# Kernel tuning notes

Hardware: AMD Instinct MI355X
Metric: run time of the kernel (lower is better)

## Reference

```python
import jax, jax.numpy as jnp
import numpy as np

B, N, E, D, R, M, L = 8, 8192, 16384, 128, 200, 20, 3


def setup_inputs() -> dict:
    key = jax.random.key(0)
    ks = jax.random.split(key, 16)
    return {
        "dists": jax.random.randint(ks[0], (B, N), 0, 10),
        "edge_index": jax.random.randint(ks[1], (B, 2, E), 0, N),
        "rels": jax.random.randint(ks[2], (B, E), 0, R),
        "node_mask": jax.random.randint(ks[3], (B, N), 0, 2).astype(bool),
        "edge_mask": jax.random.randint(ks[4], (B, E), 0, 2).astype(bool),
        "r_query_embed": jax.random.normal(ks[5], (B, D), dtype=jnp.float32),
        "conf_embeds": jax.random.normal(ks[6], (B, E, D), dtype=jnp.float32),
        "noise": jax.random.normal(ks[7], (B, N, D), dtype=jnp.float32),
        "dist_table": jax.random.normal(ks[8], (10, D), dtype=jnp.float32) * 0.02,
        "rel_table": jax.random.normal(ks[9], (R, D), dtype=jnp.float32) * 0.02,
        "msg_W": jax.random.normal(ks[10], (L, 5 * D, D), dtype=jnp.float32) / np.sqrt(5 * D),
        "msg_b": jnp.zeros((L, D), jnp.float32),
        "upd_W": jax.random.normal(ks[11], (L, D, D), dtype=jnp.float32) / np.sqrt(D),
        "upd_b": jnp.zeros((L, D), jnp.float32),
        "att_W": jax.random.normal(ks[12], (2 * D, 1), dtype=jnp.float32) / np.sqrt(2 * D),
        "att_b": jnp.zeros((1,), jnp.float32),
    }


def reference(dists, edge_index, rels, node_mask, edge_mask, r_query_embed,
              conf_embeds, noise, dist_table, rel_table, msg_W, msg_b,
              upd_W, upd_b, att_W, att_b):
    dist_emb = dist_table[jnp.clip(dists, 0, 9)]            # [B,N,D]
    h = dist_emb + noise * 0.1
    src = edge_index[:, 0, :]                               # [B,E]
    tgt = edge_index[:, 1, :]                               # [B,E]
    em = edge_mask[..., None].astype(h.dtype)               # [B,E,1]
    h_r = rel_table[rels]                                   # [B,E,D]
    dist_src = jnp.take_along_axis(dist_emb, src[..., None], axis=1)  # [B,E,D]

    def scatter_add(t_idx, msg):
        return jnp.zeros((N, D), msg.dtype).at[t_idx].add(msg)

    for k in range(L):
        h_src = jnp.take_along_axis(h, src[..., None], axis=1)        # [B,E,D]
        comp = h_src * h_r
        msg_in = jnp.concatenate([comp, h_src, dist_src, h_r, conf_embeds], axis=-1)  # [B,E,5D]
        msg = jax.nn.relu(jnp.einsum('bef,fd->bed', msg_in, msg_W[k]) + msg_b[k]) * em
        aggr = jax.vmap(scatter_add)(tgt, msg)                        # [B,N,D]
        h = jnp.einsum('bnd,df->bnf', aggr, upd_W[k]) + upd_b[k] + h

    h = h * node_mask[..., None].astype(h.dtype)
    t_state = h[:, 0, :]
    r_q = jnp.broadcast_to(r_query_embed[:, None, :], (B, N, D))
    att_in = jnp.concatenate([h, r_q], axis=-1)                       # [B,N,2D]
    scores = jax.nn.leaky_relu((att_in @ att_W + att_b)[..., 0], 0.01)
    scores = jnp.where(node_mask, scores, -1e9)
    alpha = jax.nn.softmax(scores, axis=1)
    topk_vals, topk_idx = jax.lax.top_k(alpha, M)                     # [B,M]
    H_evd = jnp.take_along_axis(h, topk_idx[..., None], axis=1) * topk_vals[..., None]
    return (H_evd, t_state)
```

## Files before the change

### kernel.cpp

```cpp
#include <hip/hip_runtime.h>
#include <hip/hip_bf16.h>
#include <math.h>

#define B_ 8
#define N_ 8192
#define E_ 16384
#define D_ 128
#define R_ 200
#define M_ 20
#define L_ 3
#define KEFF 384
#define LDA 392
#define LDU 136

typedef __attribute__((ext_vector_type(8))) short bf16x8;
typedef __attribute__((ext_vector_type(4))) float f32x4;

__device__ __forceinline__ short f2b(float f) {
  union { __hip_bfloat16 b; short s; } u;
  u.b = __float2bfloat16(f);
  return u.s;
}
__device__ __forceinline__ bf16x8 pack8(float4 x, float4 y) {
  bf16x8 r;
  r[0] = f2b(x.x); r[1] = f2b(x.y); r[2] = f2b(x.z); r[3] = f2b(x.w);
  r[4] = f2b(y.x); r[5] = f2b(y.y); r[6] = f2b(y.z); r[7] = f2b(y.w);
  return r;
}
__device__ __forceinline__ bf16x8 pack8mul(float4 x, float4 rx, float4 y, float4 ry) {
  bf16x8 r;
  r[0] = f2b(x.x * rx.x); r[1] = f2b(x.y * rx.y); r[2] = f2b(x.z * rx.z); r[3] = f2b(x.w * rx.w);
  r[4] = f2b(y.x * ry.x); r[5] = f2b(y.y * ry.y); r[6] = f2b(y.z * ry.z); r[7] = f2b(y.w * ry.w);
  return r;
}

__global__ __launch_bounds__(256) void k_init_h(const int* __restrict__ dists,
    const float* __restrict__ noise, const float* __restrict__ dist_table,
    float* __restrict__ h) {
  int i = blockIdx.x * 256 + threadIdx.x;
  int row = i >> 5;
  int d4 = i & 31;
  int dc = dists[row]; dc = dc < 0 ? 0 : (dc > 9 ? 9 : dc);
  const float4 t = *(const float4*)&dist_table[dc * D_ + d4 * 4];
  const float4 nz = *(const float4*)&noise[(size_t)i * 4];
  float4 o;
  o.x = t.x + 0.1f * nz.x; o.y = t.y + 0.1f * nz.y;
  o.z = t.z + 0.1f * nz.z; o.w = t.w + 0.1f * nz.w;
  *(float4*)&h[(size_t)i * 4] = o;
}

__global__ __launch_bounds__(256) void k_compact(const int* __restrict__ edge_mask,
    int* __restrict__ count, int* __restrict__ list) {
  int i = blockIdx.x * 256 + threadIdx.x;
  bool act = edge_mask[i] != 0;
  unsigned long long m = __ballot(act);
  int lane = threadIdx.x & 63;
  int base = 0;
  if (lane == 0) base = atomicAdd(count, __popcll(m));
  base = __shfl(base, 0);
  if (act) list[base + __popcll(m & ((1ull << lane) - 1ull))] = i;
}

__global__ __launch_bounds__(128) void k_tables(const float* __restrict__ dist_table,
    const float* __restrict__ rel_table, const float* __restrict__ msg_W,
    const float* __restrict__ msg_b, float* __restrict__ T3b, float* __restrict__ T4) {
  int k = blockIdx.x / 210;
  int r = blockIdx.x % 210;
  int d = threadIdx.x;
  if (r < 10) {
    float acc = msg_b[k * D_ + d];
    for (int f = 0; f < D_; ++f)
      acc = fmaf(dist_table[r * D_ + f], msg_W[(size_t)(k * 640 + 256 + f) * D_ + d], acc);
    T3b[(k * 10 + r) * D_ + d] = acc;
  } else {
    int rr = r - 10;
    float acc = 0.f;
    for (int f = 0; f < D_; ++f)
      acc = fmaf(rel_table[rr * D_ + f], msg_W[(size_t)(k * 640 + 384 + f) * D_ + d], acc);
    T4[(k * R_ + rr) * D_ + d] = acc;
  }
}

__global__ __launch_bounds__(256) void k_wbt_msg(const float* __restrict__ msg_W,
    short* __restrict__ Wbt) {
  int idx = blockIdx.x * 256 + threadIdx.x;
  int fe = idx % KEFF;
  int t = idx / KEFF;
  int n = t & 127;
  int k = t >> 7;
  int row = fe < 256 ? fe : fe + 256;
  Wbt[idx] = f2b(msg_W[(size_t)(k * 640 + row) * D_ + n]);
}

__global__ __launch_bounds__(256) void k_wbt_upd(const float* __restrict__ upd_W,
    short* __restrict__ Wbt) {
  int idx = blockIdx.x * 256 + threadIdx.x;
  int f = idx & 127;
  int t = idx >> 7;
  int n = t & 127;
  int k = t >> 7;
  Wbt[idx] = f2b(upd_W[(size_t)(k * D_ + f) * D_ + n]);
}

__global__ __launch_bounds__(256, 3) void k_msg(
    const int* __restrict__ count_p, const int* __restrict__ list,
    const int* __restrict__ edge_index, const int* __restrict__ rels,
    const int* __restrict__ dists, const float* __restrict__ h,
    const float* __restrict__ rel_table, const float* __restrict__ conf,
    const short* __restrict__ Wbt,
    const float* __restrict__ T3b,
    const float* __restrict__ T4,
    float* __restrict__ aggr) {
  int cnt = *count_p;
  int base = blockIdx.x * 64;
  if (base >= cnt) return;
  int ne = min(64, cnt - base);
  __shared__ __align__(16) short sA[64 * LDA];
  __shared__ int sMeta[64][5];
  int tid = threadIdx.x;
  if (tid < 64) {
    int t = tid < ne ? tid : 0;
    int id = list[base + t];
    int b = id >> 14;
    int e = id & (E_ - 1);
    int src = edge_index[(b * 2) * E_ + e];
    int tgt = edge_index[(b * 2 + 1) * E_ + e];
    int dc = dists[b * N_ + src];
    dc = dc < 0 ? 0 : (dc > 9 ? 9 : dc);
    sMeta[tid][0] = b * N_ + src;
    sMeta[tid][1] = id;
    sMeta[tid][2] = b * N_ + tgt;
    sMeta[tid][3] = dc;
    sMeta[tid][4] = rels[id];
  }
  __syncthreads();
  {
    int i = tid >> 2, q = tid & 3;
    const float4* ph = (const float4*)(h + (size_t)sMeta[i][0] * D_ + q * 32);
    const float4* pr = (const float4*)(rel_table + (size_t)sMeta[i][4] * D_ + q * 32);
    const float4* pc = (const float4*)(conf + (size_t)sMeta[i][1] * D_ + q * 32);
    float4 hv[8], rv[8], cv[8];
#pragma unroll
    for (int j = 0; j < 8; ++j) hv[j] = ph[j];
#pragma unroll
    for (int j = 0; j < 8; ++j) rv[j] = pr[j];
#pragma unroll
    for (int j = 0; j < 8; ++j) cv[j] = pc[j];
    short* rowp = &sA[i * LDA];
#pragma unroll
    for (int j = 0; j < 4; ++j) {
      *(bf16x8*)&rowp[q * 32 + j * 8]       = pack8mul(hv[2*j], rv[2*j], hv[2*j+1], rv[2*j+1]);
      *(bf16x8*)&rowp[128 + q * 32 + j * 8] = pack8(hv[2*j], hv[2*j+1]);
      *(bf16x8*)&rowp[256 + q * 32 + j * 8] = pack8(cv[2*j], cv[2*j+1]);
    }
  }
  __syncthreads();
  int lane = tid & 63, wv = tid >> 6;
  int wm = wv >> 1, wn = wv & 1;
  int g = lane >> 4, cl = lane & 15;
  const short* pa0 = &sA[(wm * 32 + cl) * LDA];
  const short* pa1 = pa0 + 16 * LDA;
  const short* wb = Wbt + (size_t)(wn * 64 + cl) * KEFF;

  f32x4 acc[2][4];
  f32x4 zz = {0.f, 0.f, 0.f, 0.f};
#pragma unroll
  for (int tm = 0; tm < 2; ++tm)
#pragma unroll
    for (int tn = 0; tn < 4; ++tn) acc[tm][tn] = zz;

#pragma unroll
  for (int kstep = 0; kstep < 12; ++kstep) {
    int o = kstep * 32 + g * 8;
    bf16x8 a0 = *(const bf16x8*)&pa0[o];
    bf16x8 a1 = *(const bf16x8*)&pa1[o];
    const short* wk = wb + o;
    bf16x8 b0 = *(const bf16x8*)(wk);
    bf16x8 b1 = *(const bf16x8*)(wk + 16 * KEFF);
    bf16x8 b2 = *(const bf16x8*)(wk + 32 * KEFF);
    bf16x8 b3 = *(const bf16x8*)(wk + 48 * KEFF);
    acc[0][0] = __builtin_amdgcn_mfma_f32_16x16x32_bf16(a0, b0, acc[0][0], 0, 0, 0);
    acc[0][1] = __builtin_amdgcn_mfma_f32_16x16x32_bf16(a0, b1, acc[0][1], 0, 0, 0);
    acc[0][2] = __builtin_amdgcn_mfma_f32_16x16x32_bf16(a0, b2, acc[0][2], 0, 0, 0);
    acc[0][3] = __builtin_amdgcn_mfma_f32_16x16x32_bf16(a0, b3, acc[0][3], 0, 0, 0);
    acc[1][0] = __builtin_amdgcn_mfma_f32_16x16x32_bf16(a1, b0, acc[1][0], 0, 0, 0);
    acc[1][1] = __builtin_amdgcn_mfma_f32_16x16x32_bf16(a1, b1, acc[1][1], 0, 0, 0);
    acc[1][2] = __builtin_amdgcn_mfma_f32_16x16x32_bf16(a1, b2, acc[1][2], 0, 0, 0);
    acc[1][3] = __builtin_amdgcn_mfma_f32_16x16x32_bf16(a1, b3, acc[1][3], 0, 0, 0);
  }
#pragma unroll
  for (int tm = 0; tm < 2; ++tm)
#pragma unroll
    for (int reg = 0; reg < 4; ++reg) {
      int edge = wm * 32 + tm * 16 + g * 4 + reg;
      if (edge < ne) {
        int arow = sMeta[edge][2];
        int dc = sMeta[edge][3];
        int rl = sMeta[edge][4];
#pragma unroll
        for (int tn = 0; tn < 4; ++tn) {
          int n = wn * 64 + tn * 16 + cl;
          float bias = T3b[dc * D_ + n] + T4[rl * D_ + n];
          float vv = fmaxf(acc[tm][tn][reg] + bias, 0.f);
          unsafeAtomicAdd(&aggr[(size_t)arow * D_ + n], vv);
        }
      }
    }
}

__global__ __launch_bounds__(256, 4) void k_upd(
    float* __restrict__ aggr, const short* __restrict__ Wbt,
    const float* __restrict__ upd_b, float* __restrict__ h) {
  int base = blockIdx.x * 64;
  int tid = threadIdx.x;
  __shared__ __align__(16) short sU[64 * LDU];
  {
    int i = tid >> 2, q = tid & 3;
    float4* ap = (float4*)(aggr + (size_t)(base + i) * D_ + q * 32);
    float4 av[8];
    float4 z4 = make_float4(0.f, 0.f, 0.f, 0.f);
#pragma unroll
    for (int j = 0; j < 8; ++j) av[j] = ap[j];
#pragma unroll
    for (int j = 0; j < 8; ++j) ap[j] = z4;
    short* rowp = &sU[i * LDU];
#pragma unroll
    for (int j = 0; j < 4; ++j)
      *(bf16x8*)&rowp[q * 32 + j * 8] = pack8(av[2*j], av[2*j+1]);
  }
  __syncthreads();
  int lane = tid & 63, wv = tid >> 6;
  int wm = wv >> 1, wn = wv & 1;
  int g = lane >> 4, cl = lane & 15;
  const short* pa0 = &sU[(wm * 32 + cl) * LDU];
  const short* pa1 = pa0 + 16 * LDU;
  const short* wb = Wbt + (size_t)(wn * 64 + cl) * D_;

  f32x4 acc[2][4];
  f32x4 zz = {0.f, 0.f, 0.f, 0.f};
#pragma unroll
  for (int tm = 0; tm < 2; ++tm)
#pragma unroll
    for (int tn = 0; tn < 4; ++tn) acc[tm][tn] = zz;

#pragma unroll
  for (int kstep = 0; kstep < 4; ++kstep) {
    int o = kstep * 32 + g * 8;
    bf16x8 a0 = *(const bf16x8*)&pa0[o];
    bf16x8 a1 = *(const bf16x8*)&pa1[o];
    const short* wk = wb + o;
    bf16x8 b0 = *(const bf16x8*)(wk);
    bf16x8 b1 = *(const bf16x8*)(wk + 16 * D_);
    bf16x8 b2 = *(const bf16x8*)(wk + 32 * D_);
    bf16x8 b3 = *(const bf16x8*)(wk + 48 * D_);
    acc[0][0] = __builtin_amdgcn_mfma_f32_16x16x32_bf16(a0, b0, acc[0][0], 0, 0, 0);
    acc[0][1] = __builtin_amdgcn_mfma_f32_16x16x32_bf16(a0, b1, acc[0][1], 0, 0, 0);
    acc[0][2] = __builtin_amdgcn_mfma_f32_16x16x32_bf16(a0, b2, acc[0][2], 0, 0, 0);
    acc[0][3] = __builtin_amdgcn_mfma_f32_16x16x32_bf16(a0, b3, acc[0][3], 0, 0, 0);
    acc[1][0] = __builtin_amdgcn_mfma_f32_16x16x32_bf16(a1, b0, acc[1][0], 0, 0, 0);
    acc[1][1] = __builtin_amdgcn_mfma_f32_16x16x32_bf16(a1, b1, acc[1][1], 0, 0, 0);
    acc[1][2] = __builtin_amdgcn_mfma_f32_16x16x32_bf16(a1, b2, acc[1][2], 0, 0, 0);
    acc[1][3] = __builtin_amdgcn_mfma_f32_16x16x32_bf16(a1, b3, acc[1][3], 0, 0, 0);
  }
#pragma unroll
  for (int tm = 0; tm < 2; ++tm)
#pragma unroll
    for (int reg = 0; reg < 4; ++reg) {
      int grow = base + wm * 32 + tm * 16 + g * 4 + reg;
#pragma unroll
      for (int tn = 0; tn < 4; ++tn) {
        int n = wn * 64 + tn * 16 + cl;
        size_t gi = (size_t)grow * D_ + n;
        h[gi] = acc[tm][tn][reg] + upd_b[n] + h[gi];
      }
    }
}

__global__ __launch_bounds__(256) void k_score(const float* __restrict__ h,
    const int* __restrict__ node_mask, const float* __restrict__ r_query,
    const float* __restrict__ att_W, const float* __restrict__ att_b,
    float* __restrict__ sSg) {
  int wv = threadIdx.x >> 6, lane = threadIdx.x & 63;
  int node = blockIdx.x * 4 + wv;
  int b = node >> 13;
  float s;
  if (node_mask[node] == 0) {
    s = -1e9f;
  } else {
    float2 hv = *(const float2*)&h[(size_t)node * D_ + lane * 2];
    float2 w0 = *(const float2*)&att_W[lane * 2];
    float2 w1 = *(const float2*)&att_W[D_ + lane * 2];
    float2 rq = *(const float2*)&r_query[b * D_ + lane * 2];
    float v = hv.x * w0.x + hv.y * w0.y + rq.x * w1.x + rq.y * w1.y;
#pragma unroll
    for (int off = 32; off > 0; off >>= 1) v += __shfl_xor(v, off);
    v += att_b[0];
    s = v > 0.f ? v : 0.01f * v;
  }
  if (lane == 0) sSg[node] = s;
}

__global__ __launch_bounds__(1024) void k_top(const float* __restrict__ sSg,
    const float* __restrict__ h, const int* __restrict__ node_mask,
    float* __restrict__ out) {
  int b = blockIdx.x;
  int tid = threadIdx.x, lane = tid & 63, wv = tid >> 6;
  __shared__ float sS[N_];
  __shared__ float sRw[16];
  __shared__ float sSegV[16];
  __shared__ int sSegI[16];
  __shared__ float sTopV[M_];
  __shared__ int sTopI[M_];
  __shared__ float sMax, sSum;
  const float4* gp = (const float4*)&sSg[(size_t)b * N_];
#pragma unroll
  for (int r = 0; r < 2; ++r) {
    float4 x = gp[tid + r * 1024];
    *(float4*)&sS[(tid + r * 1024) * 4] = x;
  }
  __syncthreads();
  float lm = -INFINITY;
  for (int n = tid; n < N_; n += 1024) lm = fmaxf(lm, sS[n]);
#pragma unroll
  for (int off = 32; off > 0; off >>= 1) lm = fmaxf(lm, __shfl_xor(lm, off));
  if (lane == 0) sRw[wv] = lm;
  __syncthreads();
  if (tid == 0) {
    float m = sRw[0];
    for (int i = 1; i < 16; ++i) m = fmaxf(m, sRw[i]);
    sMax = m;
  }
  __syncthreads();
  float mx = sMax;
  float ls = 0.f;
  for (int n = tid; n < N_; n += 1024) ls += expf(sS[n] - mx);
#pragma unroll
  for (int off = 32; off > 0; off >>= 1) ls += __shfl_xor(ls, off);
  if (lane == 0) sRw[wv] = ls;
  __syncthreads();
  if (tid == 0) {
    float s = 0.f;
    for (int i = 0; i < 16; ++i) s += sRw[i];
    sSum = s;
  }
  {
    float bv = -INFINITY; int bi = 0;
    int s0 = wv * 512;
    for (int t2 = 0; t2 < 8; ++t2) {
      int n = s0 + lane + t2 * 64;
      float x = sS[n];
      if (x > bv) { bv = x; bi = n; }
    }
#pragma unroll
    for (int off = 32; off > 0; off >>= 1) {
      float vv = __shfl_xor(bv, off); int ii = __shfl_xor(bi, off);
      if (vv > bv || (vv == bv && ii < bi)) { bv = vv; bi = ii; }
    }
    if (lane == 0) { sSegV[wv] = bv; sSegI[wv] = bi; }
  }
  __syncthreads();
  for (int j = 0; j < M_; ++j) {
    if (wv == 0) {
      float bv = (lane < 16) ? sSegV[lane] : -INFINITY;
      int bi = (lane < 16) ? sSegI[lane] : 0x7fffffff;
#pragma unroll
      for (int off = 32; off > 0; off >>= 1) {
        float vv = __shfl_xor(bv, off); int ii = __shfl_xor(bi, off);
        if (vv > bv || (vv == bv && ii < bi)) { bv = vv; bi = ii; }
      }
      if (lane == 0) { sTopV[j] = bv; sTopI[j] = bi; sS[bi] = -INFINITY; }
    }
    __syncthreads();
    int seg = sTopI[j] >> 9;
    if (wv == seg) {
      float bv = -INFINITY; int bi = 0;
      int s0 = wv * 512;
      for (int t2 = 0; t2 < 8; ++t2) {
        int n = s0 + lane + t2 * 64;
        float x = sS[n];
        if (x > bv) { bv = x; bi = n; }
      }
#pragma unroll
      for (int off = 32; off > 0; off >>= 1) {
        float vv = __shfl_xor(bv, off); int ii = __shfl_xor(bi, off);
        if (vv > bv || (vv == bv && ii < bi)) { bv = vv; bi = ii; }
      }
      if (lane == 0) { sSegV[wv] = bv; sSegI[wv] = bi; }
    }
    __syncthreads();
  }
  float sum = sSum;
  if (tid < D_) {
    float vv = node_mask[b * N_] ? h[(size_t)b * N_ * D_ + tid] : 0.f;
    out[B_ * M_ * D_ + b * D_ + tid] = vv;
  }
  for (int s2 = tid; s2 < M_ * D_; s2 += 1024) {
    int j = s2 >> 7, d = s2 & 127;
    int idx = sTopI[j];
    float alpha = expf(sTopV[j] - mx) / sum;
    float hv = h[((size_t)b * N_ + idx) * D_ + d];
    if (!node_mask[b * N_ + idx]) hv = 0.f;
    out[(b * M_ + j) * D_ + d] = hv * alpha;
  }
}

extern "C" void kernel_launch(void* const* d_in, const int* in_sizes, int n_in,
                              void* d_out, int out_size, void* d_ws, size_t ws_size,
                              hipStream_t stream) {
  const int*   dists      = (const int*)d_in[0];
  const int*   edge_index = (const int*)d_in[1];
  const int*   rels       = (const int*)d_in[2];
  const int*   node_mask  = (const int*)d_in[3];
  const int*   edge_mask  = (const int*)d_in[4];
  const float* r_query    = (const float*)d_in[5];
  const float* conf       = (const float*)d_in[6];
  const float* noise      = (const float*)d_in[7];
  const float* dist_table = (const float*)d_in[8];
  const float* rel_table  = (const float*)d_in[9];
  const float* msg_W      = (const float*)d_in[10];
  const float* msg_b      = (const float*)d_in[11];
  const float* upd_W      = (const float*)d_in[12];
  const float* upd_b      = (const float*)d_in[13];
  const float* att_W      = (const float*)d_in[14];
  const float* att_b      = (const float*)d_in[15];
  float* out = (float*)d_out;

  char* ws = (char*)d_ws;
  size_t off = 0;
  auto alloc = [&](size_t bytes) {
    void* p = ws + off;
    off = (off + bytes + 255) & ~(size_t)255;
    return p;
  };
  int*   count   = (int*)alloc(4);
  int*   list    = (int*)alloc((size_t)B_ * E_ * 4);
  float* h       = (float*)alloc((size_t)B_ * N_ * D_ * 4);
  float* aggr    = (float*)alloc((size_t)B_ * N_ * D_ * 4);
  short* Wbt_msg = (short*)alloc((size_t)L_ * D_ * KEFF * 2);
  short* Wbt_upd = (short*)alloc((size_t)L_ * D_ * D_ * 2);
  float* T3b     = (float*)alloc((size_t)L_ * 10 * D_ * 4);
  float* T4      = (float*)alloc((size_t)L_ * R_ * D_ * 4);
  float* scores  = (float*)alloc((size_t)B_ * N_ * 4);
  (void)ws_size; (void)in_sizes; (void)n_in; (void)out_size;

  hipMemsetAsync(count, 0, 4, stream);
  hipMemsetAsync(aggr, 0, (size_t)B_ * N_ * D_ * 4, stream);

  k_init_h<<<B_ * N_ * D_ / 4 / 256, 256, 0, stream>>>(dists, noise, dist_table, h);
  k_compact<<<B_ * E_ / 256, 256, 0, stream>>>(edge_mask, count, list);
  k_tables<<<L_ * 210, 128, 0, stream>>>(dist_table, rel_table, msg_W, msg_b, T3b, T4);
  k_wbt_msg<<<L_ * D_ * KEFF / 256, 256, 0, stream>>>(msg_W, Wbt_msg);
  k_wbt_upd<<<L_ * D_ * D_ / 256, 256, 0, stream>>>(upd_W, Wbt_upd);

  for (int k = 0; k < L_; ++k) {
    k_msg<<<B_ * E_ / 64, 256, 0, stream>>>(count, list, edge_index, rels, dists, h,
        rel_table, conf, Wbt_msg + (size_t)k * D_ * KEFF,
        T3b + k * 10 * D_, T4 + k * R_ * D_, aggr);
    k_upd<<<B_ * N_ / 64, 256, 0, stream>>>(aggr, Wbt_upd + (size_t)k * D_ * D_,
        upd_b + k * D_, h);
  }
  k_score<<<B_ * N_ / 4, 256, 0, stream>>>(h, node_mask, r_query, att_W, att_b, scores);
  k_top<<<B_, 1024, 0, stream>>>(scores, h, node_mask, out);
}
```

Baseline: 544.6 us.

## Replace atomic scatter-add with CSR gather of per-edge messages

Instead of each message being atomically added into a dense aggr buffer, k_msg now writes per-edge messages to a buffer. k_upd then gathers them by target node through a CSR built once, using a count, a three-kernel prefix scan and an atomic fill. This removes the float atomics and the per-layer zeroing of the 16MB aggr buffer. In exchange it writes and reads a 64MB message buffer per layer, adds several setup kernels, and gives an irregular per-thread loop over in-degree.

```diff
diff --git a/kernel.cpp b/kernel.cpp
--- a/kernel.cpp
+++ b/kernel.cpp
@@ -50,7 +50,8 @@
 }
 
 __global__ __launch_bounds__(256) void k_compact(const int* __restrict__ edge_mask,
-    int* __restrict__ count, int* __restrict__ list) {
+    const int* __restrict__ edge_index, int* __restrict__ count,
+    int* __restrict__ list, int* __restrict__ cnt) {
   int i = blockIdx.x * 256 + threadIdx.x;
   bool act = edge_mask[i] != 0;
   unsigned long long m = __ballot(act);
@@ -58,7 +59,69 @@
   int base = 0;
   if (lane == 0) base = atomicAdd(count, __popcll(m));
   base = __shfl(base, 0);
-  if (act) list[base + __popcll(m & ((1ull << lane) - 1ull))] = i;
+  if (act) {
+    list[base + __popcll(m & ((1ull << lane) - 1ull))] = i;
+    int b = i >> 14, e = i & (E_ - 1);
+    int tgt = edge_index[(b * 2 + 1) * E_ + e];
+    atomicAdd(&cnt[b * N_ + tgt], 1);
+  }
+}
+
+__global__ __launch_bounds__(256) void k_scanA(const int* __restrict__ cnt,
+    int* __restrict__ bsum) {
+  __shared__ int s[4];
+  int v = cnt[blockIdx.x * 256 + threadIdx.x];
+#pragma unroll
+  for (int o = 32; o > 0; o >>= 1) v += __shfl_xor(v, o);
+  if ((threadIdx.x & 63) == 0) s[threadIdx.x >> 6] = v;
+  __syncthreads();
+  if (threadIdx.x == 0) bsum[blockIdx.x] = s[0] + s[1] + s[2] + s[3];
+}
+
+__global__ __launch_bounds__(256) void k_scanB(const int* __restrict__ bsum,
+    int* __restrict__ boff) {
+  __shared__ int s[256];
+  int t = threadIdx.x;
+  s[t] = bsum[t];
+  __syncthreads();
+  for (int o = 1; o < 256; o <<= 1) {
+    int v = (t >= o) ? s[t - o] : 0;
+    __syncthreads();
+    s[t] += v;
+    __syncthreads();
+  }
+  boff[t] = (t == 0) ? 0 : s[t - 1];
+}
+
+__global__ __launch_bounds__(256) void k_scanC(const int* __restrict__ cnt,
+    const int* __restrict__ boff, int* __restrict__ off, int* __restrict__ cur) {
+  __shared__ int s[256];
+  int t = threadIdx.x;
+  int gi = blockIdx.x * 256 + t;
+  int v = cnt[gi];
+  s[t] = v;
+  __syncthreads();
+  for (int o = 1; o < 256; o <<= 1) {
+    int u = (t >= o) ? s[t - o] : 0;
+    __syncthreads();
+    s[t] += u;
+    __syncthreads();
+  }
+  int excl = s[t] - v + boff[blockIdx.x];
+  off[gi] = excl;
+  cur[gi] = excl;
+}
+
+__global__ __launch_bounds__(256) void k_fill(const int* __restrict__ count_p,
+    const int* __restrict__ list, const int* __restrict__ edge_index,
+    int* __restrict__ cur, int* __restrict__ csr) {
+  int j = blockIdx.x * 256 + threadIdx.x;
+  if (j >= *count_p) return;
+  int id = list[j];
+  int b = id >> 14, e = id & (E_ - 1);
+  int tgt = edge_index[(b * 2 + 1) * E_ + e];
+  int pos = atomicAdd(&cur[b * N_ + tgt], 1);
+  csr[pos] = j;
 }
 
 __global__ __launch_bounds__(128) void k_tables(const float* __restrict__ dist_table,
@@ -110,13 +173,13 @@
     const short* __restrict__ Wbt,
     const float* __restrict__ T3b,
     const float* __restrict__ T4,
-    float* __restrict__ aggr) {
+    float* __restrict__ msgbuf) {
   int cnt = *count_p;
   int base = blockIdx.x * 64;
   if (base >= cnt) return;
   int ne = min(64, cnt - base);
   __shared__ __align__(16) short sA[64 * LDA];
-  __shared__ int sMeta[64][5];
+  __shared__ int sMeta[64][4];
   int tid = threadIdx.x;
   if (tid < 64) {
     int t = tid < ne ? tid : 0;
@@ -124,20 +187,18 @@
     int b = id >> 14;
     int e = id & (E_ - 1);
     int src = edge_index[(b * 2) * E_ + e];
-    int tgt = edge_index[(b * 2 + 1) * E_ + e];
     int dc = dists[b * N_ + src];
     dc = dc < 0 ? 0 : (dc > 9 ? 9 : dc);
     sMeta[tid][0] = b * N_ + src;
     sMeta[tid][1] = id;
-    sMeta[tid][2] = b * N_ + tgt;
-    sMeta[tid][3] = dc;
-    sMeta[tid][4] = rels[id];
+    sMeta[tid][2] = dc;
+    sMeta[tid][3] = rels[id];
   }
   __syncthreads();
   {
     int i = tid >> 2, q = tid & 3;
     const float4* ph = (const float4*)(h + (size_t)sMeta[i][0] * D_ + q * 32);
-    const float4* pr = (const float4*)(rel_table + (size_t)sMeta[i][4] * D_ + q * 32);
+    const float4* pr = (const float4*)(rel_table + (size_t)sMeta[i][3] * D_ + q * 32);
     const float4* pc = (const float4*)(conf + (size_t)sMeta[i][1] * D_ + q * 32);
     float4 hv[8], rv[8], cv[8];
 #pragma unroll
@@ -194,39 +255,50 @@
     for (int reg = 0; reg < 4; ++reg) {
       int edge = wm * 32 + tm * 16 + g * 4 + reg;
       if (edge < ne) {
-        int arow = sMeta[edge][2];
-        int dc = sMeta[edge][3];
-        int rl = sMeta[edge][4];
+        int dc = sMeta[edge][2];
+        int rl = sMeta[edge][3];
+        float* mp = msgbuf + (size_t)(base + edge) * D_;
 #pragma unroll
         for (int tn = 0; tn < 4; ++tn) {
           int n = wn * 64 + tn * 16 + cl;
           float bias = T3b[dc * D_ + n] + T4[rl * D_ + n];
-          float vv = fmaxf(acc[tm][tn][reg] + bias, 0.f);
-          unsafeAtomicAdd(&aggr[(size_t)arow * D_ + n], vv);
+          mp[n] = fmaxf(acc[tm][tn][reg] + bias, 0.f);
         }
       }
     }
 }
 
 __global__ __launch_bounds__(256, 4) void k_upd(
-    float* __restrict__ aggr, const short* __restrict__ Wbt,
+    const float* __restrict__ msgbuf, const int* __restrict__ off,
+    const int* __restrict__ cnt, const int* __restrict__ csr,
+    const short* __restrict__ Wbt,
     const float* __restrict__ upd_b, float* __restrict__ h) {
   int base = blockIdx.x * 64;
   int tid = threadIdx.x;
   __shared__ __align__(16) short sU[64 * LDU];
   {
     int i = tid >> 2, q = tid & 3;
-    float4* ap = (float4*)(aggr + (size_t)(base + i) * D_ + q * 32);
-    float4 av[8];
-    float4 z4 = make_float4(0.f, 0.f, 0.f, 0.f);
-#pragma unroll
-    for (int j = 0; j < 8; ++j) av[j] = ap[j];
-#pragma unroll
-    for (int j = 0; j < 8; ++j) ap[j] = z4;
+    int node = base + i;
+    int o0 = off[node];
+    int cn = cnt[node];
+    float a[32];
+#pragma unroll
+    for (int j = 0; j < 32; ++j) a[j] = 0.f;
+    for (int p = 0; p < cn; ++p) {
+      const float4* mp = (const float4*)(msgbuf + (size_t)csr[o0 + p] * D_ + q * 32);
+#pragma unroll
+      for (int j = 0; j < 8; ++j) {
+        float4 m = mp[j];
+        a[4*j] += m.x; a[4*j+1] += m.y; a[4*j+2] += m.z; a[4*j+3] += m.w;
+      }
+    }
     short* rowp = &sU[i * LDU];
 #pragma unroll
-    for (int j = 0; j < 4; ++j)
-      *(bf16x8*)&rowp[q * 32 + j * 8] = pack8(av[2*j], av[2*j+1]);
+    for (int j = 0; j < 4; ++j) {
+      float4 x = make_float4(a[8*j], a[8*j+1], a[8*j+2], a[8*j+3]);
+      float4 y = make_float4(a[8*j+4], a[8*j+5], a[8*j+6], a[8*j+7]);
+      *(bf16x8*)&rowp[q * 32 + j * 8] = pack8(x, y);
+    }
   }
   __syncthreads();
   int lane = tid & 63, wv = tid >> 6;
@@ -426,16 +498,22 @@
   float* out = (float*)d_out;
 
   char* ws = (char*)d_ws;
-  size_t off = 0;
+  size_t off0 = 0;
   auto alloc = [&](size_t bytes) {
-    void* p = ws + off;
-    off = (off + bytes + 255) & ~(size_t)255;
+    void* p = ws + off0;
+    off0 = (off0 + bytes + 255) & ~(size_t)255;
     return p;
   };
   int*   count   = (int*)alloc(4);
   int*   list    = (int*)alloc((size_t)B_ * E_ * 4);
   float* h       = (float*)alloc((size_t)B_ * N_ * D_ * 4);
-  float* aggr    = (float*)alloc((size_t)B_ * N_ * D_ * 4);
+  float* msgbuf  = (float*)alloc((size_t)B_ * E_ * D_ * 4);
+  int*   cnt     = (int*)alloc((size_t)B_ * N_ * 4);
+  int*   offar   = (int*)alloc((size_t)B_ * N_ * 4);
+  int*   cur     = (int*)alloc((size_t)B_ * N_ * 4);
+  int*   csr     = (int*)alloc((size_t)B_ * E_ * 4);
+  int*   bsum    = (int*)alloc(256 * 4);
+  int*   boff    = (int*)alloc(256 * 4);
   short* Wbt_msg = (short*)alloc((size_t)L_ * D_ * KEFF * 2);
   short* Wbt_upd = (short*)alloc((size_t)L_ * D_ * D_ * 2);
   float* T3b     = (float*)alloc((size_t)L_ * 10 * D_ * 4);
@@ -444,10 +522,14 @@
   (void)ws_size; (void)in_sizes; (void)n_in; (void)out_size;
 
   hipMemsetAsync(count, 0, 4, stream);
-  hipMemsetAsync(aggr, 0, (size_t)B_ * N_ * D_ * 4, stream);
+  hipMemsetAsync(cnt, 0, (size_t)B_ * N_ * 4, stream);
 
   k_init_h<<<B_ * N_ * D_ / 4 / 256, 256, 0, stream>>>(dists, noise, dist_table, h);
-  k_compact<<<B_ * E_ / 256, 256, 0, stream>>>(edge_mask, count, list);
+  k_compact<<<B_ * E_ / 256, 256, 0, stream>>>(edge_mask, edge_index, count, list, cnt);
+  k_scanA<<<256, 256, 0, stream>>>(cnt, bsum);
+  k_scanB<<<1, 256, 0, stream>>>(bsum, boff);
+  k_scanC<<<256, 256, 0, stream>>>(cnt, boff, offar, cur);
+  k_fill<<<B_ * E_ / 256, 256, 0, stream>>>(count, list, edge_index, cur, csr);
   k_tables<<<L_ * 210, 128, 0, stream>>>(dist_table, rel_table, msg_W, msg_b, T3b, T4);
   k_wbt_msg<<<L_ * D_ * KEFF / 256, 256, 0, stream>>>(msg_W, Wbt_msg);
   k_wbt_upd<<<L_ * D_ * D_ / 256, 256, 0, stream>>>(upd_W, Wbt_upd);
@@ -455,9 +537,9 @@
   for (int k = 0; k < L_; ++k) {
     k_msg<<<B_ * E_ / 64, 256, 0, stream>>>(count, list, edge_index, rels, dists, h,
         rel_table, conf, Wbt_msg + (size_t)k * D_ * KEFF,
-        T3b + k * 10 * D_, T4 + k * R_ * D_, aggr);
-    k_upd<<<B_ * N_ / 64, 256, 0, stream>>>(aggr, Wbt_upd + (size_t)k * D_ * D_,
-        upd_b + k * D_, h);
+        T3b + k * 10 * D_, T4 + k * R_ * D_, msgbuf);
+    k_upd<<<B_ * N_ / 64, 256, 0, stream>>>(msgbuf, offar, cnt, csr,
+        Wbt_upd + (size_t)k * D_ * D_, upd_b + k * D_, h);
   }
   k_score<<<B_ * N_ / 4, 256, 0, stream>>>(h, node_mask, r_query, att_W, att_b, scores);
   k_top<<<B_, 1024, 0, stream>>>(scores, h, node_mask, out);
```

After: 475.2 us. 12.7% less time.
